# Kernel optimization log

Hardware: AMD Instinct MI355X
Metric: run time of the kernel (lower is better)

Reference implementation:

```python
import jax, jax.numpy as jnp
import numpy as np

B, S, D, DH = 2, 2048, 1024, 64
H = D // DH
EPS = 1e-6

def rms_norm(x):
    # flax RMSNorm, use_scale=False: x / sqrt(mean(x^2) + eps)
    return x * jax.lax.rsqrt(jnp.mean(jnp.square(x), axis=-1, keepdims=True) + EPS)

def setup_inputs() -> dict:
    key = jax.random.key(0)
    ks = jax.random.split(key, 6)
    std = (1.0 / D) ** 0.5
    x = jax.random.normal(ks[0], (B, S, D), dtype=jnp.float32)
    Wq = jax.random.normal(ks[1], (D, D), dtype=jnp.float32) * std
    Wk = jax.random.normal(ks[2], (D, D), dtype=jnp.float32) * std
    Wv = jax.random.normal(ks[3], (D, D), dtype=jnp.float32) * std
    # output_proj is zero-initialized in the original; use small random so
    # backward through it is non-trivial for kernel correctness testing.
    Wo = jax.random.normal(ks[4], (D, D), dtype=jnp.float32) * std
    mask = jnp.tril(jnp.ones((S, S), dtype=bool))[None, None]  # causal [1,1,S,S]
    return {"x": x, "Wq": Wq, "Wk": Wk, "Wv": Wv, "Wo": Wo, "mask": mask}

def reference(x, Wq, Wk, Wv, Wo, mask):
    scale = (1.0 / DH) ** 0.5
    q = (x @ Wq).reshape(B, S, H, DH).transpose(0, 2, 1, 3)  # [B,H,S,DH]
    k = (x @ Wk).reshape(B, S, H, DH).transpose(0, 2, 1, 3)
    v = (x @ Wv).reshape(B, S, H, DH).transpose(0, 2, 1, 3)
    q = rms_norm(q)
    k = rms_norm(k)
    scores = jnp.einsum('bhsd,bhtd->bhst', q, k) * scale
    scores = jnp.where(mask, scores, jnp.finfo(scores.dtype).min)
    probs = jax.nn.softmax(scores, axis=-1)
    out = jnp.einsum('bhst,bhtd->bhsd', probs, v)
    out = out.transpose(0, 2, 1, 3).reshape(B, S, D)
    return out @ Wo
```

## Files before the change

### kernel.cpp

```cpp
#include <hip/hip_runtime.h>
#include <stdint.h>


typedef __attribute__((ext_vector_type(8))) short s16x8;
typedef __attribute__((ext_vector_type(4))) float fx4;
typedef __attribute__((ext_vector_type(4))) unsigned int ux4;
typedef __attribute__((ext_vector_type(2))) unsigned int ux2;

__device__ __forceinline__ unsigned short f2bf(float x) {
  unsigned u = __builtin_bit_cast(unsigned, x);
  u += 0x7fffu + ((u >> 16) & 1u);
  return (unsigned short)(u >> 16);
}
__device__ __forceinline__ float bf2f(unsigned short h) {
  return __builtin_bit_cast(float, (unsigned)h << 16);
}

__device__ __forceinline__ void gload_lds16(const void* g, void* l) {
  __builtin_amdgcn_global_load_lds(
      (const __attribute__((address_space(1))) unsigned int*)g,
      (__attribute__((address_space(3))) unsigned int*)l, 16, 0, 0);
}

__global__ void k_conv_bf16(const float* __restrict__ X,
                            unsigned short* __restrict__ Y, int n4) {
  int stride = gridDim.x * blockDim.x;
  for (int i = blockIdx.x * blockDim.x + threadIdx.x; i < n4; i += stride) {
    fx4 v = *(const fx4*)(X + (size_t)i * 4);
    ux2 o;
    o[0] = (unsigned)f2bf(v[0]) | ((unsigned)f2bf(v[1]) << 16);
    o[1] = (unsigned)f2bf(v[2]) | ((unsigned)f2bf(v[3]) << 16);
    *(ux2*)(Y + (size_t)i * 4) = o;
  }
}

__global__ void k_transpose_w(const float* __restrict__ W0, const float* __restrict__ W1,
                              const float* __restrict__ W2, const float* __restrict__ W3,
                              unsigned short* __restrict__ T0, unsigned short* __restrict__ T1,
                              unsigned short* __restrict__ T2, unsigned short* __restrict__ T3) {
  const float* W = blockIdx.z == 0 ? W0 : blockIdx.z == 1 ? W1 : blockIdx.z == 2 ? W2 : W3;
  unsigned short* T = blockIdx.z == 0 ? T0 : blockIdx.z == 1 ? T1 : blockIdx.z == 2 ? T2 : T3;
  __shared__ float t[32][33];
  int bx = blockIdx.x * 32, by = blockIdx.y * 32;
  int tx = threadIdx.x, ty = threadIdx.y;
#pragma unroll
  for (int i = 0; i < 32; i += 8)
    t[ty + i][tx] = W[(size_t)(by + ty + i) * 1024 + bx + tx];
  __syncthreads();
#pragma unroll
  for (int i = 0; i < 32; i += 8)
    T[(size_t)(bx + ty + i) * 1024 + by + tx] = f2bf(t[tx][ty + i]);
}

template <int MODE>
__global__ __launch_bounds__(256, 2)
void k_gemm_bt(const unsigned short* __restrict__ A,
               const unsigned short* __restrict__ W0,
               const unsigned short* __restrict__ W1,
               const unsigned short* __restrict__ W2,
               void* __restrict__ Cptr, int ldc,
               unsigned short* __restrict__ qn, unsigned short* __restrict__ kn,
               unsigned short* __restrict__ vb) {
  __shared__ unsigned short As[128 * 64];
  __shared__ unsigned short Bs[128 * 64];
  const int tid = threadIdx.x;
  const int w = tid >> 6, l = tid & 63;
  const int lr = l & 15, lg = l >> 4;
  const int wm = w >> 1, wn = w & 1;
  const int m0 = blockIdx.x * 128;
  const int nt = blockIdx.y;
  const unsigned short* Bt = (nt < 8) ? W0 : (nt < 16) ? W1 : W2;
  const int n0 = (nt & 7) * 128;

  fx4 acc[4][4] = {};

  const int srow = w * 8 + (l >> 3);
  const int skb  = ((l & 7) ^ (l >> 3)) * 8;
  const unsigned short* aB = A  + (size_t)(m0 + srow) * 1024 + skb;
  const unsigned short* bB = Bt + (size_t)(n0 + srow) * 1024 + skb;
  unsigned short* aD = &As[w * 512];
  unsigned short* bD = &Bs[w * 512];
  const int rdswz = (l & 7) << 4;

  for (int kt = 0; kt < 1024; kt += 64) {
    __syncthreads();
#pragma unroll
    for (int j = 0; j < 4; ++j) {
      gload_lds16(aB + j * 32768 + kt, aD + j * 2048);
      gload_lds16(bB + j * 32768 + kt, bD + j * 2048);
    }
    __syncthreads();
#pragma unroll
    for (int ks = 0; ks < 2; ++ks) {
      const int kb = (ks * 64 + lg * 16) ^ rdswz;
      s16x8 af[4], bf[4];
#pragma unroll
      for (int mf = 0; mf < 4; ++mf)
        af[mf] = *(const s16x8*)((const char*)As + (wm * 64 + mf * 16 + lr) * 128 + kb);
#pragma unroll
      for (int nf = 0; nf < 4; ++nf)
        bf[nf] = *(const s16x8*)((const char*)Bs + (wn * 64 + nf * 16 + lr) * 128 + kb);
#pragma unroll
      for (int mf = 0; mf < 4; ++mf)
#pragma unroll
        for (int nf = 0; nf < 4; ++nf)
          acc[mf][nf] = __builtin_amdgcn_mfma_f32_16x16x32_bf16(af[mf], bf[nf], acc[mf][nf], 0, 0, 0);
    }
  }

  if (MODE == 1) {
    const int gn = nt * 128 + wn * 64;
    const int gm = m0 + wm * 64;
#pragma unroll
    for (int mf = 0; mf < 4; ++mf)
#pragma unroll
      for (int r = 0; r < 4; ++r) {
        int row = gm + mf * 16 + lg * 4 + r;
        float* C = (float*)Cptr + (size_t)row * ldc + gn;
#pragma unroll
        for (int nf = 0; nf < 4; ++nf) C[nf * 16 + lr] = acc[mf][nf][r];
      }
  } else {
    const int tz = nt >> 3;
    const int h  = ((nt & 7) << 1) | wn;
    const int gm = m0 + wm * 64;
    unsigned short* base = tz == 0 ? qn : tz == 1 ? kn : vb;
    const float cmul = (tz == 0) ? 0.18033688f : 1.0f;
#pragma unroll
    for (int mf = 0; mf < 4; ++mf)
#pragma unroll
      for (int r = 0; r < 4; ++r) {
        int m = gm + mf * 16 + lg * 4 + r;
        float ss = 0.f;
#pragma unroll
        for (int nf = 0; nf < 4; ++nf) ss += acc[mf][nf][r] * acc[mf][nf][r];
        ss += __shfl_xor(ss, 1);
        ss += __shfl_xor(ss, 2);
        ss += __shfl_xor(ss, 4);
        ss += __shfl_xor(ss, 8);
        float scale = (tz == 2) ? 1.0f : rsqrtf(ss * (1.0f / 64.0f) + 1e-6f) * cmul;
        int b = m >> 11, s = m & 2047;
        unsigned short* dst = base + ((size_t)(((b << 4) + h) * 2048 + s)) * 64;
#pragma unroll
        for (int nf = 0; nf < 4; ++nf)
          dst[nf * 16 + lr] = f2bf(acc[mf][nf][r] * scale);
      }
  }
}

__global__ __launch_bounds__(128, 2)
void k_attn(const unsigned short* __restrict__ Q,
            const unsigned short* __restrict__ K,
            const unsigned short* __restrict__ V,
            unsigned short* __restrict__ O,
            float* __restrict__ pO,
            float* __restrict__ pL) {
  __shared__ unsigned short Ks[2][64 * 64];
  __shared__ unsigned short Vt[2][64 * 64];
  __shared__ unsigned short Ps[2][32 * 64];

  const int id = blockIdx.x;
  const int bh = id >> 5;
  const int c  = id & 31;
  const int p  = c >> 1, half = c & 1;
  const int tid = threadIdx.x;
  const int w = tid >> 6, l = tid & 63;
  const int lr = l & 15, lg = l >> 4;
  const int b = bh >> 4, h = bh & 15;

  const unsigned short* Kb = K + (size_t)bh * 2048 * 64;
  const unsigned short* Vb = V + (size_t)bh * 2048 * 64;
  const unsigned short* Qh = Q + (size_t)bh * 2048 * 64;

  const int ksub = l >> 3;
  const int kskb = ((l & 7) ^ ksub) * 8;
  const int vc = tid & 31;
  const int vg = tid >> 5;
  const int kvlo = (vc & 15) + (vc >> 4) * 32;
  const int rdswz = (lr & 7) << 4;
  const float FMAX = 11.5415603f;

  const int NS = half ? 16 : 17;
  int tile = half ? (31 - p) : p;
  int qw = tile * 64 + w * 32;

  s16x8 aq[2][2];
#pragma unroll
  for (int mf = 0; mf < 2; ++mf)
#pragma unroll
    for (int ks = 0; ks < 2; ++ks)
      aq[mf][ks] = *(const s16x8*)(Qh + (size_t)(qw + mf * 16 + lr) * 64 + ks * 32 + lg * 8);

  fx4 oacc[2][4] = {};
  float lsum[2][4] = {{0.f, 0.f, 0.f, 0.f}, {0.f, 0.f, 0.f, 0.f}};

  int kvt = half ? (16 - p) : 0;

  ux4 va0, va1, va2, va3;
#pragma unroll
  for (int j = 0; j < 4; ++j)
    gload_lds16(Kb + (size_t)(kvt * 64 + j * 16 + w * 8 + ksub) * 64 + kskb,
                &Ks[0][(j * 16 + w * 8) * 64]);
  va0 = *(const ux4*)(Vb + (size_t)(kvt * 64 + kvlo) * 64 + vg * 16);
  va1 = *(const ux4*)(Vb + (size_t)(kvt * 64 + kvlo) * 64 + vg * 16 + 8);
  va2 = *(const ux4*)(Vb + (size_t)(kvt * 64 + kvlo + 16) * 64 + vg * 16);
  va3 = *(const ux4*)(Vb + (size_t)(kvt * 64 + kvlo + 16) * 64 + vg * 16 + 8);
  {
    union { ux4 v; unsigned short u[8]; } a0, a1, a2, a3;
    a0.v = va0; a1.v = va1; a2.v = va2; a3.v = va3;
#pragma unroll
    for (int i = 0; i < 8; ++i) {
      int dh = vg * 16 + i;
      *(unsigned*)((char*)&Vt[0][0] + dh * 128 + ((vc * 4) ^ ((i & 7) << 4))) =
          (unsigned)a0.u[i] | ((unsigned)a2.u[i] << 16);
      *(unsigned*)((char*)&Vt[0][0] + (dh + 8) * 128 + ((vc * 4) ^ ((i & 7) << 4))) =
          (unsigned)a1.u[i] | ((unsigned)a3.u[i] << 16);
    }
  }
  __syncthreads();

#pragma unroll 1
  for (int s = 0; s < NS; ++s) {
    if (!half && s == p + 1) {
#pragma unroll
      for (int mf = 0; mf < 2; ++mf)
#pragma unroll
        for (int r = 0; r < 4; ++r) {
          float ssum = lsum[mf][r];
          ssum += __shfl_xor(ssum, 1);
          ssum += __shfl_xor(ssum, 2);
          ssum += __shfl_xor(ssum, 4);
          ssum += __shfl_xor(ssum, 8);
          float inv = 1.0f / ssum;
          int gq = qw + mf * 16 + lg * 4 + r;
          unsigned short* orow = O + ((size_t)(b * 2048 + gq)) * 1024 + h * 64;
#pragma unroll
          for (int nf = 0; nf < 4; ++nf)
            orow[nf * 16 + lr] = f2bf(oacc[mf][nf][r] * inv);
        }
#pragma unroll
      for (int mf = 0; mf < 2; ++mf) {
#pragma unroll
        for (int nf = 0; nf < 4; ++nf) oacc[mf][nf] = fx4{0.f, 0.f, 0.f, 0.f};
#pragma unroll
        for (int r = 0; r < 4; ++r) lsum[mf][r] = 0.f;
      }
      tile = 31 - p;
      qw = tile * 64 + w * 32;
#pragma unroll
      for (int mf = 0; mf < 2; ++mf)
#pragma unroll
        for (int ks = 0; ks < 2; ++ks)
          aq[mf][ks] = *(const s16x8*)(Qh + (size_t)(qw + mf * 16 + lr) * 64 + ks * 32 + lg * 8);
    }
    const int cur = s & 1;
    const int kv0 = kvt * 64;
    const bool pre = (s + 1 < NS);
    int nkvt = kvt + 1;
    if (!half && s == p) nkvt = 0;
    if (pre) {
      const int kvn = nkvt * 64;
#pragma unroll
      for (int j = 0; j < 4; ++j)
        gload_lds16(Kb + (size_t)(kvn + j * 16 + w * 8 + ksub) * 64 + kskb,
                    &Ks[cur ^ 1][(j * 16 + w * 8) * 64]);
      va0 = *(const ux4*)(Vb + (size_t)(kvn + kvlo) * 64 + vg * 16);
      va1 = *(const ux4*)(Vb + (size_t)(kvn + kvlo) * 64 + vg * 16 + 8);
      va2 = *(const ux4*)(Vb + (size_t)(kvn + kvlo + 16) * 64 + vg * 16);
      va3 = *(const ux4*)(Vb + (size_t)(kvn + kvlo + 16) * 64 + vg * 16 + 8);
    }
    fx4 sc[2][4] = {};
    __builtin_amdgcn_s_setprio(1);
#pragma unroll
    for (int ks = 0; ks < 2; ++ks) {
      const int kb = (ks * 64 + lg * 16) ^ rdswz;
#pragma unroll
      for (int nf = 0; nf < 4; ++nf) {
        s16x8 bk = *(const s16x8*)((const char*)&Ks[cur][0] + (nf * 16 + lr) * 128 + kb);
#pragma unroll
        for (int mf = 0; mf < 2; ++mf)
          sc[mf][nf] = __builtin_amdgcn_mfma_f32_16x16x32_bf16(aq[mf][ks], bk, sc[mf][nf], 0, 0, 0);
      }
    }
    __builtin_amdgcn_s_setprio(0);
    const bool diag = half ? (s == 15) : (s == p);
    if (diag) {
#pragma unroll
      for (int mf = 0; mf < 2; ++mf)
#pragma unroll
        for (int nf = 0; nf < 4; ++nf)
#pragma unroll
          for (int r = 0; r < 4; ++r) {
            int gq = qw + mf * 16 + lg * 4 + r;
            int gk = kv0 + nf * 16 + lr;
            if (gk > gq) sc[mf][nf][r] = -3.0e38f;
          }
    }
    char* pw = (char*)&Ps[w][0];
#pragma unroll
    for (int mf = 0; mf < 2; ++mf)
#pragma unroll
      for (int r = 0; r < 4; ++r) {
        float p0 = __builtin_amdgcn_exp2f(sc[mf][0][r] - FMAX);
        float p1 = __builtin_amdgcn_exp2f(sc[mf][1][r] - FMAX);
        float p2 = __builtin_amdgcn_exp2f(sc[mf][2][r] - FMAX);
        float p3 = __builtin_amdgcn_exp2f(sc[mf][3][r] - FMAX);
        lsum[mf][r] += (p0 + p1) + (p2 + p3);
        int row = mf * 16 + lg * 4 + r;
        char* pb = pw + row * 128;
        int swz = (row & 7) << 4;
        *(unsigned*)(pb + ((4 * lr) ^ swz))      = (unsigned)f2bf(p0) | ((unsigned)f2bf(p1) << 16);
        *(unsigned*)(pb + ((64 + 4 * lr) ^ swz)) = (unsigned)f2bf(p2) | ((unsigned)f2bf(p3) << 16);
      }
    __builtin_amdgcn_s_setprio(1);
#pragma unroll
    for (int ks = 0; ks < 2; ++ks) {
      s16x8 pa[2], bv[4];
#pragma unroll
      for (int mf = 0; mf < 2; ++mf) {
        int row = mf * 16 + lr;
        pa[mf] = *(const s16x8*)(pw + row * 128 + ((ks * 64 + lg * 16) ^ ((row & 7) << 4)));
      }
#pragma unroll
      for (int nf = 0; nf < 4; ++nf) {
        int row = nf * 16 + lr;
        bv[nf] = *(const s16x8*)((const char*)&Vt[cur][0] + row * 128 +
                                 ((ks * 64 + lg * 16) ^ ((row & 7) << 4)));
      }
#pragma unroll
      for (int mf = 0; mf < 2; ++mf)
#pragma unroll
        for (int nf = 0; nf < 4; ++nf)
          oacc[mf][nf] = __builtin_amdgcn_mfma_f32_16x16x32_bf16(pa[mf], bv[nf], oacc[mf][nf], 0, 0, 0);
    }
    __builtin_amdgcn_s_setprio(0);
    if (pre) {
      union { ux4 v; unsigned short u[8]; } a0, a1, a2, a3;
      a0.v = va0; a1.v = va1; a2.v = va2; a3.v = va3;
#pragma unroll
      for (int i = 0; i < 8; ++i) {
        int dh = vg * 16 + i;
        *(unsigned*)((char*)&Vt[cur ^ 1][0] + dh * 128 + ((vc * 4) ^ ((i & 7) << 4))) =
            (unsigned)a0.u[i] | ((unsigned)a2.u[i] << 16);
        *(unsigned*)((char*)&Vt[cur ^ 1][0] + (dh + 8) * 128 + ((vc * 4) ^ ((i & 7) << 4))) =
            (unsigned)a1.u[i] | ((unsigned)a3.u[i] << 16);
      }
    }
    kvt = nkvt;
    __syncthreads();
  }

  const int slot = ((bh * 16 + p) * 2 + half);
#pragma unroll
  for (int mf = 0; mf < 2; ++mf)
#pragma unroll
    for (int r = 0; r < 4; ++r) {
      float ssum = lsum[mf][r];
      ssum += __shfl_xor(ssum, 1);
      ssum += __shfl_xor(ssum, 2);
      ssum += __shfl_xor(ssum, 4);
      ssum += __shfl_xor(ssum, 8);
      int row = w * 32 + mf * 16 + lg * 4 + r;
      float* po = pO + ((size_t)slot * 64 + row) * 64;
#pragma unroll
      for (int nf = 0; nf < 4; ++nf) po[nf * 16 + lr] = oacc[mf][nf][r];
      if (lr == 0) pL[slot * 64 + row] = ssum;
    }
}

__global__ __launch_bounds__(256)
void k_merge(const float* __restrict__ pO, const float* __restrict__ pL,
             unsigned short* __restrict__ O) {
  int gid = blockIdx.x * 256 + threadIdx.x;
  int row = gid >> 4;
  int quad = gid & 15;
  int slot = row >> 6;
  int r = row & 63;
  int bh = slot >> 4, p = slot & 15;
  fx4 va = *(const fx4*)(pO + ((size_t)(slot * 2) * 64 + r) * 64 + quad * 4);
  fx4 vb = *(const fx4*)(pO + ((size_t)(slot * 2 + 1) * 64 + r) * 64 + quad * 4);
  float inv = 1.0f / (pL[(slot * 2) * 64 + r] + pL[(slot * 2 + 1) * 64 + r]);
  int tile = 31 - p;
  int b = bh >> 4, h = bh & 15;
  int s = tile * 64 + r;
  unsigned short* o = O + ((size_t)(b * 2048 + s)) * 1024 + h * 64 + quad * 4;
  ux2 out;
  out[0] = (unsigned)f2bf((va[0] + vb[0]) * inv) | ((unsigned)f2bf((va[1] + vb[1]) * inv) << 16);
  out[1] = (unsigned)f2bf((va[2] + vb[2]) * inv) | ((unsigned)f2bf((va[3] + vb[3]) * inv) << 16);
  *(ux2*)o = out;
}

extern "C" void kernel_launch(void* const* d_in, const int* in_sizes, int n_in,
                              void* d_out, int out_size, void* d_ws, size_t ws_size,
                              hipStream_t stream) {
  const float* x  = (const float*)d_in[0];
  const float* Wq = (const float*)d_in[1];
  const float* Wk = (const float*)d_in[2];
  const float* Wv = (const float*)d_in[3];
  const float* Wo = (const float*)d_in[4];

  char* ws = (char*)d_ws;
  unsigned short* xb   = (unsigned short*)(ws);
  unsigned short* WqT  = (unsigned short*)(ws + (8ll  << 20));
  unsigned short* WkT  = (unsigned short*)(ws + (10ll << 20));
  unsigned short* WvT  = (unsigned short*)(ws + (12ll << 20));
  unsigned short* WoT  = (unsigned short*)(ws + (14ll << 20));
  unsigned short* qn   = (unsigned short*)(ws + (16ll << 20));
  unsigned short* kn   = (unsigned short*)(ws + (24ll << 20));
  unsigned short* vb   = (unsigned short*)(ws + (32ll << 20));
  unsigned short* attn = (unsigned short*)(ws + (40ll << 20));
  float* pO            = (float*)(ws + (48ll << 20));
  float* pL            = (float*)(ws + (64ll << 20));

  k_conv_bf16<<<1024, 256, 0, stream>>>(x, xb, 4096 * 1024 / 4);
  k_transpose_w<<<dim3(32, 32, 4), dim3(32, 8), 0, stream>>>(Wq, Wk, Wv, Wo, WqT, WkT, WvT, WoT);
  k_gemm_bt<2><<<dim3(32, 24), 256, 0, stream>>>(xb, WqT, WkT, WvT, nullptr, 0, qn, kn, vb);
  k_attn<<<1024, 128, 0, stream>>>(qn, kn, vb, attn, pO, pL);
  k_merge<<<2048, 256, 0, stream>>>(pO, pL, attn);
  k_gemm_bt<1><<<dim3(32, 8), 256, 0, stream>>>(attn, WoT, WoT, WoT, d_out, 1024, nullptr, nullptr, nullptr);
}
```

Before: 110.9 us.

## Software-pipeline QK of next tile with softmax/PV of current tile

Restructures the attention loop so that QK^T for the next KV tile is computed before softmax and PV of the current tile. K is now prefetched two tiles ahead and V one tile ahead, and the loop is unrolled by two with ping-pong score registers. It also replaces the manual bf16 rounding with the packed v_cvt_pk_bf16_f32 instruction. The aim is to overlap MFMA work with exp and LDS traffic and to hide load latency, at the cost of more register pressure from two score sets.

```diff
diff --git a/kernel.cpp b/kernel.cpp
--- a/kernel.cpp
+++ b/kernel.cpp
@@ -184,44 +184,155 @@
   int tile = half ? (31 - p) : p;
   int qw = tile * 64 + w * 32;
 
+  auto kvtOf = [&](int s) -> int {
+    if (half) return 16 - p + s;
+    return (s <= p) ? s : (s - p - 1);
+  };
+
   s16x8 aq[2][2];
-#pragma unroll
-  for (int mf = 0; mf < 2; ++mf)
-#pragma unroll
-    for (int ks = 0; ks < 2; ++ks)
-      aq[mf][ks] = *(const s16x8*)(Qh + (size_t)(qw + mf * 16 + lr) * 64 + ks * 32 + lg * 8);
+  auto loadAQ = [&]() {
+#pragma unroll
+    for (int mf = 0; mf < 2; ++mf)
+#pragma unroll
+      for (int ks = 0; ks < 2; ++ks)
+        aq[mf][ks] = *(const s16x8*)(Qh + (size_t)(qw + mf * 16 + lr) * 64 + ks * 32 + lg * 8);
+  };
+  loadAQ();
 
   fx4 oacc[2][4] = {};
   float lsum[2][4] = {{0.f, 0.f, 0.f, 0.f}, {0.f, 0.f, 0.f, 0.f}};
 
-  int kvt = half ? (16 - p) : 0;
-
+  auto issueK = [&](int s, int buf) {
+    const int kv0 = kvtOf(s) * 64;
+#pragma unroll
+    for (int j = 0; j < 4; ++j)
+      gload_lds16(Kb + (size_t)(kv0 + j * 16 + w * 8 + ksub) * 64 + kskb,
+                  &Ks[buf][(j * 16 + w * 8) * 64]);
+  };
   ux4 va0, va1, va2, va3;
-#pragma unroll
-  for (int j = 0; j < 4; ++j)
-    gload_lds16(Kb + (size_t)(kvt * 64 + j * 16 + w * 8 + ksub) * 64 + kskb,
-                &Ks[0][(j * 16 + w * 8) * 64]);
-  va0 = *(const ux4*)(Vb + (size_t)(kvt * 64 + kvlo) * 64 + vg * 16);
-  va1 = *(const ux4*)(Vb + (size_t)(kvt * 64 + kvlo) * 64 + vg * 16 + 8);
-  va2 = *(const ux4*)(Vb + (size_t)(kvt * 64 + kvlo + 16) * 64 + vg * 16);
-  va3 = *(const ux4*)(Vb + (size_t)(kvt * 64 + kvlo + 16) * 64 + vg * 16 + 8);
-  {
+  auto loadV = [&](int s) {
+    const int kv0 = kvtOf(s) * 64;
+    va0 = *(const ux4*)(Vb + (size_t)(kv0 + kvlo) * 64 + vg * 16);
+    va1 = *(const ux4*)(Vb + (size_t)(kv0 + kvlo) * 64 + vg * 16 + 8);
+    va2 = *(const ux4*)(Vb + (size_t)(kv0 + kvlo + 16) * 64 + vg * 16);
+    va3 = *(const ux4*)(Vb + (size_t)(kv0 + kvlo + 16) * 64 + vg * 16 + 8);
+  };
+  auto writeV = [&](int buf) {
     union { ux4 v; unsigned short u[8]; } a0, a1, a2, a3;
     a0.v = va0; a1.v = va1; a2.v = va2; a3.v = va3;
 #pragma unroll
     for (int i = 0; i < 8; ++i) {
       int dh = vg * 16 + i;
-      *(unsigned*)((char*)&Vt[0][0] + dh * 128 + ((vc * 4) ^ ((i & 7) << 4))) =
+      *(unsigned*)((char*)&Vt[buf][0] + dh * 128 + ((vc * 4) ^ ((i & 7) << 4))) =
           (unsigned)a0.u[i] | ((unsigned)a2.u[i] << 16);
-      *(unsigned*)((char*)&Vt[0][0] + (dh + 8) * 128 + ((vc * 4) ^ ((i & 7) << 4))) =
+      *(unsigned*)((char*)&Vt[buf][0] + (dh + 8) * 128 + ((vc * 4) ^ ((i & 7) << 4))) =
           (unsigned)a1.u[i] | ((unsigned)a3.u[i] << 16);
     }
-  }
+  };
+  auto qk = [&](fx4 (&sc)[2][4], int buf) {
+#pragma unroll
+    for (int mf = 0; mf < 2; ++mf)
+#pragma unroll
+      for (int nf = 0; nf < 4; ++nf) sc[mf][nf] = fx4{0.f, 0.f, 0.f, 0.f};
+    __builtin_amdgcn_s_setprio(1);
+#pragma unroll
+    for (int ks = 0; ks < 2; ++ks) {
+      const int kb = (ks * 64 + lg * 16) ^ rdswz;
+#pragma unroll
+      for (int nf = 0; nf < 4; ++nf) {
+        s16x8 bk = *(const s16x8*)((const char*)&Ks[buf][0] + (nf * 16 + lr) * 128 + kb);
+#pragma unroll
+        for (int mf = 0; mf < 2; ++mf)
+          sc[mf][nf] = __builtin_amdgcn_mfma_f32_16x16x32_bf16(aq[mf][ks], bk, sc[mf][nf], 0, 0, 0);
+      }
+    }
+    __builtin_amdgcn_s_setprio(0);
+  };
+  auto maskDiag = [&](fx4 (&sc)[2][4], int kv0) {
+#pragma unroll
+    for (int mf = 0; mf < 2; ++mf)
+#pragma unroll
+      for (int nf = 0; nf < 4; ++nf)
+#pragma unroll
+        for (int r = 0; r < 4; ++r) {
+          int gq = qw + mf * 16 + lg * 4 + r;
+          int gk = kv0 + nf * 16 + lr;
+          if (gk > gq) sc[mf][nf][r] = -3.0e38f;
+        }
+  };
+  auto smPV = [&](fx4 (&sc)[2][4], int vbuf) {
+    char* pw = (char*)&Ps[w][0];
+#pragma unroll
+    for (int mf = 0; mf < 2; ++mf)
+#pragma unroll
+      for (int r = 0; r < 4; ++r) {
+        float e0 = __builtin_amdgcn_exp2f(sc[mf][0][r] - FMAX);
+        float e1 = __builtin_amdgcn_exp2f(sc[mf][1][r] - FMAX);
+        float e2 = __builtin_amdgcn_exp2f(sc[mf][2][r] - FMAX);
+        float e3 = __builtin_amdgcn_exp2f(sc[mf][3][r] - FMAX);
+        lsum[mf][r] += (e0 + e1) + (e2 + e3);
+        unsigned u01, u23;
+        asm("v_cvt_pk_bf16_f32 %0, %1, %2" : "=v"(u01) : "v"(e0), "v"(e1));
+        asm("v_cvt_pk_bf16_f32 %0, %1, %2" : "=v"(u23) : "v"(e2), "v"(e3));
+        int row = mf * 16 + lg * 4 + r;
+        char* pb = pw + row * 128;
+        int swz = (row & 7) << 4;
+        *(unsigned*)(pb + ((4 * lr) ^ swz)) = u01;
+        *(unsigned*)(pb + ((64 + 4 * lr) ^ swz)) = u23;
+      }
+    __builtin_amdgcn_s_setprio(1);
+#pragma unroll
+    for (int ks = 0; ks < 2; ++ks) {
+      s16x8 pa[2], bv[4];
+#pragma unroll
+      for (int mf = 0; mf < 2; ++mf) {
+        int row = mf * 16 + lr;
+        pa[mf] = *(const s16x8*)(pw + row * 128 + ((ks * 64 + lg * 16) ^ ((row & 7) << 4)));
+      }
+#pragma unroll
+      for (int nf = 0; nf < 4; ++nf) {
+        int row = nf * 16 + lr;
+        bv[nf] = *(const s16x8*)((const char*)&Vt[vbuf][0] + row * 128 +
+                                 ((ks * 64 + lg * 16) ^ ((row & 7) << 4)));
+      }
+#pragma unroll
+      for (int mf = 0; mf < 2; ++mf)
+#pragma unroll
+        for (int nf = 0; nf < 4; ++nf)
+          oacc[mf][nf] = __builtin_amdgcn_mfma_f32_16x16x32_bf16(pa[mf], bv[nf], oacc[mf][nf], 0, 0, 0);
+    }
+    __builtin_amdgcn_s_setprio(0);
+  };
+
+  issueK(0, 0);
+  issueK(1, 1);
+  loadV(0);
+  writeV(0);
+  loadV(1);
   __syncthreads();
 
-#pragma unroll 1
-  for (int s = 0; s < NS; ++s) {
-    if (!half && s == p + 1) {
+  fx4 scA[2][4], scB[2][4];
+  qk(scA, 0);
+  if (!half && p == 0) maskDiag(scA, 0);
+
+  auto body = [&](fx4 (&scP)[2][4], fx4 (&scN)[2][4], int t) {
+    const bool hasN1 = (t + 1 < NS);
+    const bool hasN2 = (t + 2 < NS);
+    if (hasN2) issueK(t + 2, t & 1);
+    if (hasN1) {
+      if (!half && (t + 1 == p + 1)) {
+        tile = 31 - p;
+        qw = tile * 64 + w * 32;
+        loadAQ();
+      }
+      qk(scN, (t + 1) & 1);
+      if ((!half && t + 1 == p) || (half && t + 1 == 15))
+        maskDiag(scN, kvtOf(t + 1) * 64);
+    }
+    if (hasN1) writeV((t + 1) & 1);
+    if (hasN2) loadV(t + 2);
+    smPV(scP, t & 1);
+    if (!half && t == p) {
 #pragma unroll
       for (int mf = 0; mf < 2; ++mf)
 #pragma unroll
@@ -232,7 +343,7 @@
           ssum += __shfl_xor(ssum, 4);
           ssum += __shfl_xor(ssum, 8);
           float inv = 1.0f / ssum;
-          int gq = qw + mf * 16 + lg * 4 + r;
+          int gq = p * 64 + w * 32 + mf * 16 + lg * 4 + r;
           unsigned short* orow = O + ((size_t)(b * 2048 + gq)) * 1024 + h * 64;
 #pragma unroll
           for (int nf = 0; nf < 4; ++nf)
@@ -245,109 +356,14 @@
 #pragma unroll
         for (int r = 0; r < 4; ++r) lsum[mf][r] = 0.f;
       }
-      tile = 31 - p;
-      qw = tile * 64 + w * 32;
-#pragma unroll
-      for (int mf = 0; mf < 2; ++mf)
-#pragma unroll
-        for (int ks = 0; ks < 2; ++ks)
-          aq[mf][ks] = *(const s16x8*)(Qh + (size_t)(qw + mf * 16 + lr) * 64 + ks * 32 + lg * 8);
-    }
-    const int cur = s & 1;
-    const int kv0 = kvt * 64;
-    const bool pre = (s + 1 < NS);
-    int nkvt = kvt + 1;
-    if (!half && s == p) nkvt = 0;
-    if (pre) {
-      const int kvn = nkvt * 64;
-#pragma unroll
-      for (int j = 0; j < 4; ++j)
-        gload_lds16(Kb + (size_t)(kvn + j * 16 + w * 8 + ksub) * 64 + kskb,
-                    &Ks[cur ^ 1][(j * 16 + w * 8) * 64]);
-      va0 = *(const ux4*)(Vb + (size_t)(kvn + kvlo) * 64 + vg * 16);
-      va1 = *(const ux4*)(Vb + (size_t)(kvn + kvlo) * 64 + vg * 16 + 8);
-      va2 = *(const ux4*)(Vb + (size_t)(kvn + kvlo + 16) * 64 + vg * 16);
-      va3 = *(const ux4*)(Vb + (size_t)(kvn + kvlo + 16) * 64 + vg * 16 + 8);
-    }
-    fx4 sc[2][4] = {};
-    __builtin_amdgcn_s_setprio(1);
-#pragma unroll
-    for (int ks = 0; ks < 2; ++ks) {
-      const int kb = (ks * 64 + lg * 16) ^ rdswz;
-#pragma unroll
-      for (int nf = 0; nf < 4; ++nf) {
-        s16x8 bk = *(const s16x8*)((const char*)&Ks[cur][0] + (nf * 16 + lr) * 128 + kb);
-#pragma unroll
-        for (int mf = 0; mf < 2; ++mf)
-          sc[mf][nf] = __builtin_amdgcn_mfma_f32_16x16x32_bf16(aq[mf][ks], bk, sc[mf][nf], 0, 0, 0);
-      }
-    }
-    __builtin_amdgcn_s_setprio(0);
-    const bool diag = half ? (s == 15) : (s == p);
-    if (diag) {
-#pragma unroll
-      for (int mf = 0; mf < 2; ++mf)
-#pragma unroll
-        for (int nf = 0; nf < 4; ++nf)
-#pragma unroll
-          for (int r = 0; r < 4; ++r) {
-            int gq = qw + mf * 16 + lg * 4 + r;
-            int gk = kv0 + nf * 16 + lr;
-            if (gk > gq) sc[mf][nf][r] = -3.0e38f;
-          }
-    }
-    char* pw = (char*)&Ps[w][0];
-#pragma unroll
-    for (int mf = 0; mf < 2; ++mf)
-#pragma unroll
-      for (int r = 0; r < 4; ++r) {
-        float p0 = __builtin_amdgcn_exp2f(sc[mf][0][r] - FMAX);
-        float p1 = __builtin_amdgcn_exp2f(sc[mf][1][r] - FMAX);
-        float p2 = __builtin_amdgcn_exp2f(sc[mf][2][r] - FMAX);
-        float p3 = __builtin_amdgcn_exp2f(sc[mf][3][r] - FMAX);
-        lsum[mf][r] += (p0 + p1) + (p2 + p3);
-        int row = mf * 16 + lg * 4 + r;
-        char* pb = pw + row * 128;
-        int swz = (row & 7) << 4;
-        *(unsigned*)(pb + ((4 * lr) ^ swz))      = (unsigned)f2bf(p0) | ((unsigned)f2bf(p1) << 16);
-        *(unsigned*)(pb + ((64 + 4 * lr) ^ swz)) = (unsigned)f2bf(p2) | ((unsigned)f2bf(p3) << 16);
-      }
-    __builtin_amdgcn_s_setprio(1);
-#pragma unroll
-    for (int ks = 0; ks < 2; ++ks) {
-      s16x8 pa[2], bv[4];
-#pragma unroll
-      for (int mf = 0; mf < 2; ++mf) {
-        int row = mf * 16 + lr;
-        pa[mf] = *(const s16x8*)(pw + row * 128 + ((ks * 64 + lg * 16) ^ ((row & 7) << 4)));
-      }
-#pragma unroll
-      for (int nf = 0; nf < 4; ++nf) {
-        int row = nf * 16 + lr;
-        bv[nf] = *(const s16x8*)((const char*)&Vt[cur][0] + row * 128 +
-                                 ((ks * 64 + lg * 16) ^ ((row & 7) << 4)));
-      }
-#pragma unroll
-      for (int mf = 0; mf < 2; ++mf)
-#pragma unroll
-        for (int nf = 0; nf < 4; ++nf)
-          oacc[mf][nf] = __builtin_amdgcn_mfma_f32_16x16x32_bf16(pa[mf], bv[nf], oacc[mf][nf], 0, 0, 0);
-    }
-    __builtin_amdgcn_s_setprio(0);
-    if (pre) {
-      union { ux4 v; unsigned short u[8]; } a0, a1, a2, a3;
-      a0.v = va0; a1.v = va1; a2.v = va2; a3.v = va3;
-#pragma unroll
-      for (int i = 0; i < 8; ++i) {
-        int dh = vg * 16 + i;
-        *(unsigned*)((char*)&Vt[cur ^ 1][0] + dh * 128 + ((vc * 4) ^ ((i & 7) << 4))) =
-            (unsigned)a0.u[i] | ((unsigned)a2.u[i] << 16);
-        *(unsigned*)((char*)&Vt[cur ^ 1][0] + (dh + 8) * 128 + ((vc * 4) ^ ((i & 7) << 4))) =
-            (unsigned)a1.u[i] | ((unsigned)a3.u[i] << 16);
-      }
-    }
-    kvt = nkvt;
+    }
     __syncthreads();
+  };
+
+#pragma unroll 1
+  for (int t = 0; t < NS; t += 2) {
+    body(scA, scB, t);
+    if (t + 1 < NS) body(scB, scA, t + 1);
   }
 
   const int slot = ((bh * 16 + p) * 2 + half);
```

Result: slower. 138.3 us (+24.8%).
